# Kernel tuning notes

Measured on AMD Instinct MI355X. Metric: run time of the kernel, lower is better.

Reference implementation:

```python
import jax, jax.numpy as jnp
import numpy as np

B, N, D = 2, 2048, 1024
H, DH = 16, 64
EPS = 1e-5


def _layernorm(t, g, b):
    m = jnp.mean(t, axis=-1, keepdims=True)
    v = jnp.mean(jnp.square(t - m), axis=-1, keepdims=True)
    return (t - m) * jax.lax.rsqrt(v + EPS) * g + b


def setup_inputs() -> dict:
    key = jax.random.key(0)
    ks = jax.random.split(key, 4)
    return {
        "x": jax.random.normal(ks[0], (B, N, D), dtype=jnp.float32),
        "ln_g": jnp.ones((D,), jnp.float32),
        "ln_b": jnp.zeros((D,), jnp.float32),
        "lnc_g": jnp.ones((D,), jnp.float32),
        "lnc_b": jnp.zeros((D,), jnp.float32),
        "Wq": jax.random.normal(ks[1], (D, H * DH), jnp.float32) * 0.02,
        "Wkv": jax.random.normal(ks[2], (D, 2 * H * DH), jnp.float32) * 0.02,
        "Wo": jax.random.normal(ks[3], (H * DH, D), jnp.float32) * 0.02,
    }


def reference(x, ln_g, ln_b, lnc_g, lnc_b, Wq, Wkv, Wo):
    scale = DH ** (-0.5)
    xn = _layernorm(x, ln_g, ln_b)          # self-attn: context = x
    cn = _layernorm(x, lnc_g, lnc_b)
    q = xn @ Wq                              # [b, n, h*d]
    kv = cn @ Wkv
    k, v = jnp.split(kv, 2, axis=-1)
    # b n (h d) -> b h n d
    q = q.reshape(B, N, H, DH).transpose(0, 2, 1, 3)
    k = k.reshape(B, N, H, DH).transpose(0, 2, 1, 3)
    v = v.reshape(B, N, H, DH).transpose(0, 2, 1, 3)
    sim = jnp.einsum("bhnd,bhmd->bhnm", q, k) * scale
    neg = -jnp.finfo(sim.dtype).max
    causal = jnp.tril(jnp.ones((N, N), dtype=bool))  # allow j <= i
    sim = jnp.where(causal[None, None], sim, neg)
    attn = jax.nn.softmax(sim.astype(jnp.float32), axis=-1)
    out = jnp.einsum("bhnm,bhmd->bhnd", attn, v)
    out = out.transpose(0, 2, 1, 3).reshape(B, N, H * DH)
    return out @ Wo
```

## Files before the change

### kernel.cpp

```cpp
#include <hip/hip_runtime.h>
#include <hip/hip_bf16.h>

#define B_  2
#define N_  2048
#define D_  1024
#define H_  16
#define DH_ 64
#define BN_ROWS (B_ * N_)
#define EPS_ 1e-5f
#define QKV_N 3072

typedef __attribute__((ext_vector_type(8))) short bf16x8_t;
typedef __attribute__((ext_vector_type(4))) float f32x4_t;

typedef const unsigned int __attribute__((address_space(1)))* gas_ptr;
typedef unsigned int __attribute__((address_space(3)))* las_ptr;

__device__ __forceinline__ void async16(const unsigned short* g, unsigned short* l) {
    __builtin_amdgcn_global_load_lds((gas_ptr)g, (las_ptr)l, 16, 0, 0);
}

__device__ __forceinline__ unsigned short f2bf(float f) {
    unsigned int u = __float_as_uint(f);
    unsigned int r = u + 0x7FFFu + ((u >> 16) & 1u);
    return (unsigned short)(r >> 16);
}

__device__ __forceinline__ unsigned int pk2bf(float a, float b) {
    __hip_bfloat162 t = __float22bfloat162_rn(float2{a, b});
    return *(unsigned int*)&t;
}

__global__ __launch_bounds__(256) void ln_wt_kernel(
    const float* __restrict__ x,
    const float* __restrict__ g1, const float* __restrict__ b1,
    const float* __restrict__ g2, const float* __restrict__ b2,
    const float* __restrict__ Wq, const float* __restrict__ Wkv,
    const float* __restrict__ Wo,
    unsigned short* __restrict__ xn, unsigned short* __restrict__ cn,
    unsigned short* __restrict__ wqkvT, unsigned short* __restrict__ woT) {
    const int bid = blockIdx.x;
    const int tid = threadIdx.x;

    if (bid < BN_ROWS) {
        const int row = bid;
        const float4 v = ((const float4*)(x + (size_t)row * D_))[tid];

        float s  = v.x + v.y + v.z + v.w;
        float s2 = v.x * v.x + v.y * v.y + v.z * v.z + v.w * v.w;
        #pragma unroll
        for (int off = 32; off > 0; off >>= 1) {
            s  += __shfl_down(s,  off);
            s2 += __shfl_down(s2, off);
        }
        __shared__ float red[8];
        if ((tid & 63) == 0) { red[tid >> 6] = s; red[4 + (tid >> 6)] = s2; }
        __syncthreads();
        const float S  = red[0] + red[1] + red[2] + red[3];
        const float S2 = red[4] + red[5] + red[6] + red[7];
        const float mean = S * (1.0f / D_);
        const float var  = S2 * (1.0f / D_) - mean * mean;
        const float rstd = rsqrtf(var + EPS_);

        const float4 G1 = ((const float4*)g1)[tid];
        const float4 B1 = ((const float4*)b1)[tid];
        const float4 G2 = ((const float4*)g2)[tid];
        const float4 B2 = ((const float4*)b2)[tid];

        float nx[4] = { (v.x - mean) * rstd, (v.y - mean) * rstd,
                        (v.z - mean) * rstd, (v.w - mean) * rstd };
        ushort4 o1, o2;
        o1.x = f2bf(nx[0] * G1.x + B1.x); o1.y = f2bf(nx[1] * G1.y + B1.y);
        o1.z = f2bf(nx[2] * G1.z + B1.z); o1.w = f2bf(nx[3] * G1.w + B1.w);
        o2.x = f2bf(nx[0] * G2.x + B2.x); o2.y = f2bf(nx[1] * G2.y + B2.y);
        o2.z = f2bf(nx[2] * G2.z + B2.z); o2.w = f2bf(nx[3] * G2.w + B2.w);
        ((ushort4*)(xn + (size_t)row * D_))[tid] = o1;
        ((ushort4*)(cn + (size_t)row * D_))[tid] = o2;
    } else {
        const int zz = bid - BN_ROWS;
        const float* src;
        unsigned short* dst;
        int N, t;
        if (zz < 1024)      { src = Wq;  dst = wqkvT;                       N = 1024; t = zz; }
        else if (zz < 3072) { src = Wkv; dst = wqkvT + (size_t)1024 * 1024; N = 2048; t = zz - 1024; }
        else                { src = Wo;  dst = woT;                         N = 1024; t = zz - 3072; }
        const int nb = N / 32;
        const int n0 = (t % nb) * 32, k0 = (t / nb) * 32;

        __shared__ float tile[32][33];
        const int tx = tid & 31, ty = tid >> 5;
        #pragma unroll
        for (int i = 0; i < 4; i++)
            tile[ty + i * 8][tx] = src[(size_t)(k0 + ty + i * 8) * N + n0 + tx];
        __syncthreads();
        #pragma unroll
        for (int i = 0; i < 4; i++)
            dst[(size_t)(n0 + ty + i * 8) * 1024 + k0 + tx] = f2bf(tile[tx][ty + i * 8]);
    }
}

template <int BM, bool FUSED, bool BF16OUT, int MINW>
__global__ __launch_bounds__(256, MINW) void gemm_kernel(
    const unsigned short* __restrict__ A0, const unsigned short* __restrict__ A1,
    const unsigned short* __restrict__ Bt, void* __restrict__ Cv,
    unsigned short* __restrict__ vt, int M, int N, int K) {
    constexpr int WM = BM / 2, MT = WM / 16, AI = BM / 32;
    __shared__ unsigned short As[BM * 64];
    __shared__ unsigned short Bs[128 * 64];
    const int tid = threadIdx.x, lane = tid & 63, w = tid >> 6;
    const int quad = lane >> 4, l16 = lane & 15;
    const int lr8 = lane >> 3, pg8 = lane & 7;
    const int wr = (w >> 1) * WM, wc = (w & 1) * 64;
    const int bm = blockIdx.y * BM, bn = blockIdx.x * 128;
    const unsigned short* A = (FUSED && bn >= 1024) ? A1 : A0;
    const float cscale = (FUSED && bn < 1024) ? 0.180336880111120f : 1.0f;

    f32x4_t acc[MT][4] = {};
    for (int k0 = 0; k0 < K; k0 += 64) {
        #pragma unroll
        for (int i = 0; i < AI; i++) {
            const int rb = w * (BM / 4) + i * 8;
            const int r  = rb + lr8;
            const int g  = pg8 ^ (r & 7);
            async16(&A[(size_t)(bm + r) * K + k0 + g * 8], &As[rb * 64]);
        }
        #pragma unroll
        for (int i = 0; i < 4; i++) {
            const int rb = w * 32 + i * 8;
            const int r  = rb + lr8;
            const int g  = pg8 ^ (r & 7);
            async16(&Bt[(size_t)(bn + r) * K + k0 + g * 8], &Bs[rb * 64]);
        }
        __syncthreads();
        #pragma unroll
        for (int kk = 0; kk < 64; kk += 32) {
            bf16x8_t af[MT], bfr[4];
            const int g0 = (kk >> 3) + quad;
            #pragma unroll
            for (int t = 0; t < MT; t++)
                af[t] = *(const bf16x8_t*)&As[(wr + t * 16 + l16) * 64 +
                                              ((g0 ^ (l16 & 7)) * 8)];
            #pragma unroll
            for (int t = 0; t < 4; t++)
                bfr[t] = *(const bf16x8_t*)&Bs[(wc + t * 16 + l16) * 64 +
                                               ((g0 ^ (l16 & 7)) * 8)];
            #pragma unroll
            for (int mt = 0; mt < MT; mt++)
                #pragma unroll
                for (int nt = 0; nt < 4; nt++)
                    acc[mt][nt] = __builtin_amdgcn_mfma_f32_16x16x32_bf16(
                        af[mt], bfr[nt], acc[mt][nt], 0, 0, 0);
        }
        __syncthreads();
    }

    if (FUSED && bn >= 2048) {
        const int seq0 = bm + wr;
        const int bq = seq0 >> 11;
        const int kt = (seq0 & (N_ - 1)) >> 6;
        #pragma unroll
        for (int nt = 0; nt < 4; nt++) {
            const int c = (bn - 2048) + wc + nt * 16 + l16;
            unsigned short* dst =
                vt + (((size_t)(bq * 32 + kt) * 1024) + c) * 64;
            #pragma unroll
            for (int mt = 0; mt < 4; mt++) {
                uint2 v2 = { pk2bf(acc[mt][nt][0], acc[mt][nt][1]),
                             pk2bf(acc[mt][nt][2], acc[mt][nt][3]) };
                *(uint2*)&dst[mt * 16 + quad * 4] = v2;
            }
        }
        return;
    }

    #pragma unroll
    for (int mt = 0; mt < MT; mt++)
        #pragma unroll
        for (int nt = 0; nt < 4; nt++)
            #pragma unroll
            for (int r = 0; r < 4; r++) {
                const int row = bm + wr + mt * 16 + quad * 4 + r;
                const int col = bn + wc + nt * 16 + l16;
                if (BF16OUT)
                    ((unsigned short*)Cv)[(size_t)row * N + col] =
                        f2bf(acc[mt][nt][r] * cscale);
                else
                    ((float*)Cv)[(size_t)row * N + col] = acc[mt][nt][r];
            }
}

__global__ __launch_bounds__(256, 3) void flash_attn_kernel(
    const unsigned short* __restrict__ qkv, const unsigned short* __restrict__ vt,
    unsigned short* __restrict__ out) {
    __shared__ unsigned short Qs[64 * 64];
    __shared__ unsigned short Ks[2][64 * 64];
    __shared__ unsigned short Vts[2][64 * 64];
    __shared__ unsigned short Ps[4][16 * 72];

    const int tid = threadIdx.x, lane = tid & 63, w = tid >> 6;
    const int quad = lane >> 4, l16 = lane & 15;
    const int lr8 = lane >> 3, pg8 = lane & 7;
    const int bid = blockIdx.x;
    const int b5  = bid & 31;
    const int bh  = (b5 & 7) * 4 + (b5 >> 3);
    const int qt  = 31 - (bid >> 5);
    const int b = bh >> 4, h = bh & 15;
    const int qs = qt * 64;
    const int niter = qt + 1;

    const unsigned short* qb  = qkv + (size_t)(b * N_) * QKV_N + h * DH_;
    const unsigned short* kb  = qb + 1024;
    const unsigned short* vtb = vt + ((size_t)(b * 32) * 1024 + h * 64) * 64;

    bf16x8_t ones;
    #pragma unroll
    for (int j = 0; j < 8; j++) ones[j] = (short)0x3F80;

    const int r0 = w * 16 + lr8;
    const int r1 = r0 + 8;
    const int g0s = pg8 ^ (r0 & 7);
    const int g1s = pg8 ^ (r1 & 7);
    const unsigned short* kp0 = &kb[(size_t)r0 * QKV_N + g0s * 8];
    const unsigned short* kp1 = &kb[(size_t)r1 * QKV_N + g1s * 8];
    const unsigned short* vp0 = &vtb[(size_t)r0 * 64 + g0s * 8];
    const unsigned short* vp1 = &vtb[(size_t)r1 * 64 + g1s * 8];
    const int rb0 = w * 16, rb1 = w * 16 + 8;

    async16(&qb[(size_t)(qs + r0) * QKV_N + g0s * 8], &Qs[rb0 * 64]);
    async16(&qb[(size_t)(qs + r1) * QKV_N + g1s * 8], &Qs[rb1 * 64]);
    async16(kp0, &Ks[0][rb0 * 64]);
    async16(kp1, &Ks[0][rb1 * 64]);
    async16(vp0, &Vts[0][rb0 * 64]);
    async16(vp1, &Vts[0][rb1 * 64]);
    __syncthreads();

    bf16x8_t qf[2];
    #pragma unroll
    for (int k2 = 0; k2 < 2; k2++) {
        const int gq = k2 * 4 + quad;
        qf[k2] = *(const bf16x8_t*)&Qs[(w * 16 + l16) * 64 + ((gq ^ (l16 & 7)) * 8)];
    }

    int ksoff[2][4], vtoff[2][4], psoff[2];
    #pragma unroll
    for (int k2 = 0; k2 < 2; k2++) {
        const int gq = k2 * 4 + quad;
        #pragma unroll
        for (int t = 0; t < 4; t++) {
            ksoff[k2][t] = (t * 16 + l16) * 64 + ((gq ^ (l16 & 7)) * 8);
            vtoff[k2][t] = ksoff[k2][t];
        }
        psoff[k2] = l16 * 72 + k2 * 32 + quad * 8;
    }
    const int qy = qs + w * 16 + l16;

    f32x4_t o[4] = {};
    f32x4_t lacc = {};

    for (int jt = 0; jt < niter; jt++) {
        if (jt) __syncthreads();

        if (jt + 1 < niter) {
            const size_t koff = (size_t)(jt + 1) * 64 * QKV_N;
            const size_t voff = (size_t)(jt + 1) * 1024 * 64;
            const int bsel = (jt + 1) & 1;
            async16(kp0 + koff, &Ks[bsel][rb0 * 64]);
            async16(kp1 + koff, &Ks[bsel][rb1 * 64]);
            async16(vp0 + voff, &Vts[bsel][rb0 * 64]);
            async16(vp1 + voff, &Vts[bsel][rb1 * 64]);
        }
        const int buf = jt & 1;
        const int js = jt * 64;

        f32x4_t s[4] = {};
        #pragma unroll
        for (int k2 = 0; k2 < 2; k2++)
            #pragma unroll
            for (int kt = 0; kt < 4; kt++) {
                const bf16x8_t a = *(const bf16x8_t*)&Ks[buf][ksoff[k2][kt]];
                s[kt] = __builtin_amdgcn_mfma_f32_16x16x32_bf16(
                    a, qf[k2], s[kt], 0, 0, 0);
            }

        const bool edge = (jt == niter - 1);
        #pragma unroll
        for (int kt = 0; kt < 4; kt++) {
            float p[4];
            #pragma unroll
            for (int r = 0; r < 4; r++) {
                float sv = s[kt][r];
                if (edge && (js + kt * 16 + quad * 4 + r > qy)) sv = -3e38f;
                p[r] = exp2f(sv);
            }
            uint2 pk = { pk2bf(p[0], p[1]), pk2bf(p[2], p[3]) };
            *(uint2*)&Ps[w][l16 * 72 + kt * 16 + quad * 4] = pk;
        }

        #pragma unroll
        for (int k2 = 0; k2 < 2; k2++) {
            const bf16x8_t ap = *(const bf16x8_t*)&Ps[w][psoff[k2]];
            #pragma unroll
            for (int nt = 0; nt < 4; nt++) {
                const bf16x8_t bv = *(const bf16x8_t*)&Vts[buf][vtoff[k2][nt]];
                o[nt] = __builtin_amdgcn_mfma_f32_16x16x32_bf16(
                    ap, bv, o[nt], 0, 0, 0);
            }
            lacc = __builtin_amdgcn_mfma_f32_16x16x32_bf16(
                ap, ones, lacc, 0, 0, 0);
        }
    }

    #pragma unroll
    for (int r = 0; r < 4; r++) {
        const float inv = 1.0f / lacc[r];
        const int query = qs + w * 16 + quad * 4 + r;
        const int row = b * N_ + query;
        #pragma unroll
        for (int nt = 0; nt < 4; nt++) {
            const int col = h * DH_ + nt * 16 + l16;
            out[(size_t)row * (H_ * DH_) + col] = f2bf(o[nt][r] * inv);
        }
    }
}

extern "C" void kernel_launch(void* const* d_in, const int* in_sizes, int n_in,
                              void* d_out, int out_size, void* d_ws, size_t ws_size,
                              hipStream_t stream) {
    const float* x     = (const float*)d_in[0];
    const float* ln_g  = (const float*)d_in[1];
    const float* ln_b  = (const float*)d_in[2];
    const float* lnc_g = (const float*)d_in[3];
    const float* lnc_b = (const float*)d_in[4];
    const float* Wq    = (const float*)d_in[5];
    const float* Wkv   = (const float*)d_in[6];
    const float* Wo    = (const float*)d_in[7];

    char* ws = (char*)d_ws;
    const size_t MB = 1024 * 1024;
    unsigned short* qkv   = (unsigned short*)(ws + 0 * MB);
    unsigned short* vtbuf = (unsigned short*)(ws + 24 * MB);
    unsigned short* xn    = (unsigned short*)(ws + 32 * MB);
    unsigned short* cn    = (unsigned short*)(ws + 40 * MB);
    unsigned short* wqkvT = (unsigned short*)(ws + 48 * MB);
    unsigned short* woT   = (unsigned short*)(ws + 54 * MB);
    unsigned short* ao    = xn;

    ln_wt_kernel<<<8192, 256, 0, stream>>>(
        x, ln_g, ln_b, lnc_g, lnc_b, Wq, Wkv, Wo, xn, cn, wqkvT, woT);

    gemm_kernel<128, true, true, 3>
        <<<dim3(QKV_N / 128, BN_ROWS / 128), 256, 0, stream>>>(
        xn, cn, wqkvT, qkv, vtbuf, BN_ROWS, QKV_N, D_);

    flash_attn_kernel<<<B_ * H_ * 32, 256, 0, stream>>>(qkv, vtbuf, ao);

    gemm_kernel<64, false, false, 2>
        <<<dim3(D_ / 128, BN_ROWS / 64), 256, 0, stream>>>(
        ao, nullptr, woT, (float*)d_out, nullptr, BN_ROWS, D_, H_ * DH_);
}
```

Measured before the change: 182.8 us.

## Pair complementary causal query tiles per block to balance work and share K/V

Each attention block now handles two query tiles, p and 31-p, so every block does roughly the same number of causal key iterations and each K/V tile loaded into LDS serves both query tiles. The grid is halved, the P scratch buffer is aliased onto the Q staging area after the Q fragments are moved to registers, and launch bounds drop to 2 blocks per SM. This removes the causal tail imbalance and halves K/V loads per query, in exchange for more registers (two accumulator sets) and fewer resident blocks.

Result: slower. 190.5 us (+4.2%).

```diff
diff --git a/kernel.cpp b/kernel.cpp
--- a/kernel.cpp
+++ b/kernel.cpp
@@ -189,13 +189,12 @@
             }
 }
 
-__global__ __launch_bounds__(256, 3) void flash_attn_kernel(
+__global__ __launch_bounds__(256, 2) void flash_attn_kernel(
     const unsigned short* __restrict__ qkv, const unsigned short* __restrict__ vt,
     unsigned short* __restrict__ out) {
-    __shared__ unsigned short Qs[64 * 64];
+    __shared__ unsigned short Qs[2][64 * 64];
     __shared__ unsigned short Ks[2][64 * 64];
     __shared__ unsigned short Vts[2][64 * 64];
-    __shared__ unsigned short Ps[4][16 * 72];
 
     const int tid = threadIdx.x, lane = tid & 63, w = tid >> 6;
     const int quad = lane >> 4, l16 = lane & 15;
@@ -203,10 +202,11 @@
     const int bid = blockIdx.x;
     const int b5  = bid & 31;
     const int bh  = (b5 & 7) * 4 + (b5 >> 3);
-    const int qt  = 31 - (bid >> 5);
+    const int p   = bid >> 5;
     const int b = bh >> 4, h = bh & 15;
-    const int qs = qt * 64;
-    const int niter = qt + 1;
+    const int qtA = p, qtB = 31 - p;
+    const int qsA = qtA * 64, qsB = qtB * 64;
+    const int niter = qtB + 1;
 
     const unsigned short* qb  = qkv + (size_t)(b * N_) * QKV_N + h * DH_;
     const unsigned short* kb  = qb + 1024;
@@ -216,46 +216,45 @@
     #pragma unroll
     for (int j = 0; j < 8; j++) ones[j] = (short)0x3F80;
 
-    const int r0 = w * 16 + lr8;
-    const int r1 = r0 + 8;
-    const int g0s = pg8 ^ (r0 & 7);
-    const int g1s = pg8 ^ (r1 & 7);
+    const int r0 = w * 16 + lr8, r1 = r0 + 8;
+    const int g0s = pg8 ^ (r0 & 7), g1s = pg8 ^ (r1 & 7);
+    const int rb0 = w * 16, rb1 = rb0 + 8;
     const unsigned short* kp0 = &kb[(size_t)r0 * QKV_N + g0s * 8];
     const unsigned short* kp1 = &kb[(size_t)r1 * QKV_N + g1s * 8];
     const unsigned short* vp0 = &vtb[(size_t)r0 * 64 + g0s * 8];
     const unsigned short* vp1 = &vtb[(size_t)r1 * 64 + g1s * 8];
-    const int rb0 = w * 16, rb1 = w * 16 + 8;
-
-    async16(&qb[(size_t)(qs + r0) * QKV_N + g0s * 8], &Qs[rb0 * 64]);
-    async16(&qb[(size_t)(qs + r1) * QKV_N + g1s * 8], &Qs[rb1 * 64]);
+
+    async16(&qb[(size_t)(qsA + r0) * QKV_N + g0s * 8], &Qs[0][rb0 * 64]);
+    async16(&qb[(size_t)(qsA + r1) * QKV_N + g1s * 8], &Qs[0][rb1 * 64]);
+    async16(&qb[(size_t)(qsB + r0) * QKV_N + g0s * 8], &Qs[1][rb0 * 64]);
+    async16(&qb[(size_t)(qsB + r1) * QKV_N + g1s * 8], &Qs[1][rb1 * 64]);
     async16(kp0, &Ks[0][rb0 * 64]);
     async16(kp1, &Ks[0][rb1 * 64]);
     async16(vp0, &Vts[0][rb0 * 64]);
     async16(vp1, &Vts[0][rb1 * 64]);
     __syncthreads();
 
-    bf16x8_t qf[2];
+    bf16x8_t qfA[2], qfB[2];
+    int fragoff[2][4], psoff[2];
     #pragma unroll
     for (int k2 = 0; k2 < 2; k2++) {
         const int gq = k2 * 4 + quad;
-        qf[k2] = *(const bf16x8_t*)&Qs[(w * 16 + l16) * 64 + ((gq ^ (l16 & 7)) * 8)];
-    }
-
-    int ksoff[2][4], vtoff[2][4], psoff[2];
-    #pragma unroll
-    for (int k2 = 0; k2 < 2; k2++) {
-        const int gq = k2 * 4 + quad;
-        #pragma unroll
-        for (int t = 0; t < 4; t++) {
-            ksoff[k2][t] = (t * 16 + l16) * 64 + ((gq ^ (l16 & 7)) * 8);
-            vtoff[k2][t] = ksoff[k2][t];
-        }
+        const int qo = (w * 16 + l16) * 64 + ((gq ^ (l16 & 7)) * 8);
+        qfA[k2] = *(const bf16x8_t*)&Qs[0][qo];
+        qfB[k2] = *(const bf16x8_t*)&Qs[1][qo];
+        #pragma unroll
+        for (int t = 0; t < 4; t++)
+            fragoff[k2][t] = (t * 16 + l16) * 64 + ((gq ^ (l16 & 7)) * 8);
         psoff[k2] = l16 * 72 + k2 * 32 + quad * 8;
     }
-    const int qy = qs + w * 16 + l16;
-
-    f32x4_t o[4] = {};
-    f32x4_t lacc = {};
+    __syncthreads();
+
+    unsigned short* Psw = &Qs[0][0] + w * (16 * 72);
+    const int qyA = qsA + w * 16 + l16;
+    const int qyB = qsB + w * 16 + l16;
+
+    f32x4_t oA[4] = {}, oB[4] = {};
+    f32x4_t lA = {}, lB = {};
 
     for (int jt = 0; jt < niter; jt++) {
         if (jt) __syncthreads();
@@ -271,54 +270,97 @@
         }
         const int buf = jt & 1;
         const int js = jt * 64;
-
-        f32x4_t s[4] = {};
+        const bool actA = (jt <= p);
+
+        f32x4_t sA[4] = {}, sB[4] = {};
+        if (actA) {
+            #pragma unroll
+            for (int k2 = 0; k2 < 2; k2++)
+                #pragma unroll
+                for (int kt = 0; kt < 4; kt++) {
+                    const bf16x8_t a = *(const bf16x8_t*)&Ks[buf][fragoff[k2][kt]];
+                    sB[kt] = __builtin_amdgcn_mfma_f32_16x16x32_bf16(a, qfB[k2], sB[kt], 0, 0, 0);
+                    sA[kt] = __builtin_amdgcn_mfma_f32_16x16x32_bf16(a, qfA[k2], sA[kt], 0, 0, 0);
+                }
+        } else {
+            #pragma unroll
+            for (int k2 = 0; k2 < 2; k2++)
+                #pragma unroll
+                for (int kt = 0; kt < 4; kt++) {
+                    const bf16x8_t a = *(const bf16x8_t*)&Ks[buf][fragoff[k2][kt]];
+                    sB[kt] = __builtin_amdgcn_mfma_f32_16x16x32_bf16(a, qfB[k2], sB[kt], 0, 0, 0);
+                }
+        }
+
+        bf16x8_t bv[2][4];
         #pragma unroll
         for (int k2 = 0; k2 < 2; k2++)
             #pragma unroll
+            for (int nt = 0; nt < 4; nt++)
+                bv[k2][nt] = *(const bf16x8_t*)&Vts[buf][fragoff[k2][nt]];
+
+        {
+            const bool edge = (jt == qtB);
+            #pragma unroll
             for (int kt = 0; kt < 4; kt++) {
-                const bf16x8_t a = *(const bf16x8_t*)&Ks[buf][ksoff[k2][kt]];
-                s[kt] = __builtin_amdgcn_mfma_f32_16x16x32_bf16(
-                    a, qf[k2], s[kt], 0, 0, 0);
-            }
-
-        const bool edge = (jt == niter - 1);
-        #pragma unroll
-        for (int kt = 0; kt < 4; kt++) {
-            float p[4];
-            #pragma unroll
-            for (int r = 0; r < 4; r++) {
-                float sv = s[kt][r];
-                if (edge && (js + kt * 16 + quad * 4 + r > qy)) sv = -3e38f;
-                p[r] = exp2f(sv);
-            }
-            uint2 pk = { pk2bf(p[0], p[1]), pk2bf(p[2], p[3]) };
-            *(uint2*)&Ps[w][l16 * 72 + kt * 16 + quad * 4] = pk;
-        }
-
-        #pragma unroll
-        for (int k2 = 0; k2 < 2; k2++) {
-            const bf16x8_t ap = *(const bf16x8_t*)&Ps[w][psoff[k2]];
-            #pragma unroll
-            for (int nt = 0; nt < 4; nt++) {
-                const bf16x8_t bv = *(const bf16x8_t*)&Vts[buf][vtoff[k2][nt]];
-                o[nt] = __builtin_amdgcn_mfma_f32_16x16x32_bf16(
-                    ap, bv, o[nt], 0, 0, 0);
-            }
-            lacc = __builtin_amdgcn_mfma_f32_16x16x32_bf16(
-                ap, ones, lacc, 0, 0, 0);
+                float pv[4];
+                #pragma unroll
+                for (int r = 0; r < 4; r++) {
+                    float sv = sB[kt][r];
+                    if (edge && (js + kt * 16 + quad * 4 + r > qyB)) sv = -3e38f;
+                    pv[r] = exp2f(sv);
+                }
+                uint2 pk = { pk2bf(pv[0], pv[1]), pk2bf(pv[2], pv[3]) };
+                *(uint2*)&Psw[l16 * 72 + kt * 16 + quad * 4] = pk;
+            }
+            #pragma unroll
+            for (int k2 = 0; k2 < 2; k2++) {
+                const bf16x8_t ap = *(const bf16x8_t*)&Psw[psoff[k2]];
+                #pragma unroll
+                for (int nt = 0; nt < 4; nt++)
+                    oB[nt] = __builtin_amdgcn_mfma_f32_16x16x32_bf16(
+                        ap, bv[k2][nt], oB[nt], 0, 0, 0);
+                lB = __builtin_amdgcn_mfma_f32_16x16x32_bf16(ap, ones, lB, 0, 0, 0);
+            }
+        }
+
+        if (actA) {
+            const bool edge = (jt == qtA);
+            #pragma unroll
+            for (int kt = 0; kt < 4; kt++) {
+                float pv[4];
+                #pragma unroll
+                for (int r = 0; r < 4; r++) {
+                    float sv = sA[kt][r];
+                    if (edge && (js + kt * 16 + quad * 4 + r > qyA)) sv = -3e38f;
+                    pv[r] = exp2f(sv);
+                }
+                uint2 pk = { pk2bf(pv[0], pv[1]), pk2bf(pv[2], pv[3]) };
+                *(uint2*)&Psw[l16 * 72 + kt * 16 + quad * 4] = pk;
+            }
+            #pragma unroll
+            for (int k2 = 0; k2 < 2; k2++) {
+                const bf16x8_t ap = *(const bf16x8_t*)&Psw[psoff[k2]];
+                #pragma unroll
+                for (int nt = 0; nt < 4; nt++)
+                    oA[nt] = __builtin_amdgcn_mfma_f32_16x16x32_bf16(
+                        ap, bv[k2][nt], oA[nt], 0, 0, 0);
+                lA = __builtin_amdgcn_mfma_f32_16x16x32_bf16(ap, ones, lA, 0, 0, 0);
+            }
         }
     }
 
     #pragma unroll
     for (int r = 0; r < 4; r++) {
-        const float inv = 1.0f / lacc[r];
-        const int query = qs + w * 16 + quad * 4 + r;
-        const int row = b * N_ + query;
+        const float invA = 1.0f / lA[r];
+        const float invB = 1.0f / lB[r];
+        const int rowA = b * N_ + qsA + w * 16 + quad * 4 + r;
+        const int rowB = b * N_ + qsB + w * 16 + quad * 4 + r;
         #pragma unroll
         for (int nt = 0; nt < 4; nt++) {
             const int col = h * DH_ + nt * 16 + l16;
-            out[(size_t)row * (H_ * DH_) + col] = f2bf(o[nt][r] * inv);
+            out[(size_t)rowA * (H_ * DH_) + col] = f2bf(oA[nt][r] * invA);
+            out[(size_t)rowB * (H_ * DH_) + col] = f2bf(oB[nt][r] * invB);
         }
     }
 }
@@ -352,7 +394,7 @@
         <<<dim3(QKV_N / 128, BN_ROWS / 128), 256, 0, stream>>>(
         xn, cn, wqkvT, qkv, vtbuf, BN_ROWS, QKV_N, D_);
 
-    flash_attn_kernel<<<B_ * H_ * 32, 256, 0, stream>>>(qkv, vtbuf, ao);
+    flash_attn_kernel<<<B_ * H_ * 16, 256, 0, stream>>>(qkv, vtbuf, ao);
 
     gemm_kernel<64, false, false, 2>
         <<<dim3(D_ / 128, BN_ROWS / 64), 256, 0, stream>>>(
```

## Enlarge flash-attention query tile to 128 rows per block with balanced scheduling

Applied to the files above, without the earlier changes.

Each attention block now handles 128 query rows instead of 64, and each wave computes two 16-row query fragments, so every K/V tile loaded into LDS and every K/V fragment read is reused across twice as many queries. The grid halves to 512 blocks, and the block-to-tile mapping pairs short and long causal rows (qt = a or 15-a) to balance work. It gives up occupancy (launch bounds 3 to 2, larger LDS and register footprint) and applies masking over two diagonal iterations instead of one.

Measured after the change: 201.2 us. 1.1x slower.

```diff
diff --git a/kernel.cpp b/kernel.cpp
--- a/kernel.cpp
+++ b/kernel.cpp
@@ -189,24 +189,26 @@
             }
 }
 
-__global__ __launch_bounds__(256, 3) void flash_attn_kernel(
+__global__ __launch_bounds__(256, 2) void flash_attn_kernel(
     const unsigned short* __restrict__ qkv, const unsigned short* __restrict__ vt,
     unsigned short* __restrict__ out) {
-    __shared__ unsigned short Qs[64 * 64];
+    __shared__ unsigned short Qs[128 * 64];
     __shared__ unsigned short Ks[2][64 * 64];
     __shared__ unsigned short Vts[2][64 * 64];
-    __shared__ unsigned short Ps[4][16 * 72];
+    __shared__ unsigned short Ps[4][32 * 72];
 
     const int tid = threadIdx.x, lane = tid & 63, w = tid >> 6;
     const int quad = lane >> 4, l16 = lane & 15;
     const int lr8 = lane >> 3, pg8 = lane & 7;
+
     const int bid = blockIdx.x;
-    const int b5  = bid & 31;
-    const int bh  = (b5 & 7) * 4 + (b5 >> 3);
-    const int qt  = 31 - (bid >> 5);
+    const int c   = bid & 255, hi = bid >> 8;
+    const int bh  = (c & 7) * 4 + ((c >> 3) & 3);
+    const int a   = c >> 5;
+    const int qt  = hi ? (15 - a) : a;
     const int b = bh >> 4, h = bh & 15;
-    const int qs = qt * 64;
-    const int niter = qt + 1;
+    const int qs = qt * 128;
+    const int niter = 2 * qt + 2;
 
     const unsigned short* qb  = qkv + (size_t)(b * N_) * QKV_N + h * DH_;
     const unsigned short* kb  = qb + 1024;
@@ -216,46 +218,44 @@
     #pragma unroll
     for (int j = 0; j < 8; j++) ones[j] = (short)0x3F80;
 
-    const int r0 = w * 16 + lr8;
-    const int r1 = r0 + 8;
-    const int g0s = pg8 ^ (r0 & 7);
-    const int g1s = pg8 ^ (r1 & 7);
+    const int r0 = w * 16 + lr8, r1 = r0 + 8;
+    const int g0s = pg8 ^ (r0 & 7), g1s = pg8 ^ (r1 & 7);
+    const int rb0 = w * 16, rb1 = rb0 + 8;
     const unsigned short* kp0 = &kb[(size_t)r0 * QKV_N + g0s * 8];
     const unsigned short* kp1 = &kb[(size_t)r1 * QKV_N + g1s * 8];
     const unsigned short* vp0 = &vtb[(size_t)r0 * 64 + g0s * 8];
     const unsigned short* vp1 = &vtb[(size_t)r1 * 64 + g1s * 8];
-    const int rb0 = w * 16, rb1 = w * 16 + 8;
-
-    async16(&qb[(size_t)(qs + r0) * QKV_N + g0s * 8], &Qs[rb0 * 64]);
-    async16(&qb[(size_t)(qs + r1) * QKV_N + g1s * 8], &Qs[rb1 * 64]);
+
+    #pragma unroll
+    for (int i = 0; i < 4; i++) {
+        const int rb = w * 32 + i * 8;
+        const int r  = rb + lr8;
+        const int g  = pg8 ^ (r & 7);
+        async16(&qb[(size_t)(qs + r) * QKV_N + g * 8], &Qs[rb * 64]);
+    }
     async16(kp0, &Ks[0][rb0 * 64]);
     async16(kp1, &Ks[0][rb1 * 64]);
     async16(vp0, &Vts[0][rb0 * 64]);
     async16(vp1, &Vts[0][rb1 * 64]);
     __syncthreads();
 
-    bf16x8_t qf[2];
+    bf16x8_t qf[2][2];
+    int fragoff[2][4], psoff[2];
     #pragma unroll
     for (int k2 = 0; k2 < 2; k2++) {
         const int gq = k2 * 4 + quad;
-        qf[k2] = *(const bf16x8_t*)&Qs[(w * 16 + l16) * 64 + ((gq ^ (l16 & 7)) * 8)];
-    }
-
-    int ksoff[2][4], vtoff[2][4], psoff[2];
-    #pragma unroll
-    for (int k2 = 0; k2 < 2; k2++) {
-        const int gq = k2 * 4 + quad;
-        #pragma unroll
-        for (int t = 0; t < 4; t++) {
-            ksoff[k2][t] = (t * 16 + l16) * 64 + ((gq ^ (l16 & 7)) * 8);
-            vtoff[k2][t] = ksoff[k2][t];
-        }
+        #pragma unroll
+        for (int nq = 0; nq < 2; nq++)
+            qf[nq][k2] = *(const bf16x8_t*)&Qs[
+                (w * 32 + nq * 16 + l16) * 64 + ((gq ^ (l16 & 7)) * 8)];
+        #pragma unroll
+        for (int t = 0; t < 4; t++)
+            fragoff[k2][t] = (t * 16 + l16) * 64 + ((gq ^ (l16 & 7)) * 8);
         psoff[k2] = l16 * 72 + k2 * 32 + quad * 8;
     }
-    const int qy = qs + w * 16 + l16;
-
-    f32x4_t o[4] = {};
-    f32x4_t lacc = {};
+
+    f32x4_t o[2][4] = {};
+    f32x4_t lacc[2] = {};
 
     for (int jt = 0; jt < niter; jt++) {
         if (jt) __syncthreads();
@@ -272,55 +272,70 @@
         const int buf = jt & 1;
         const int js = jt * 64;
 
-        f32x4_t s[4] = {};
+        f32x4_t s[4][2] = {};
         #pragma unroll
         for (int k2 = 0; k2 < 2; k2++)
             #pragma unroll
             for (int kt = 0; kt < 4; kt++) {
-                const bf16x8_t a = *(const bf16x8_t*)&Ks[buf][ksoff[k2][kt]];
-                s[kt] = __builtin_amdgcn_mfma_f32_16x16x32_bf16(
-                    a, qf[k2], s[kt], 0, 0, 0);
-            }
-
-        const bool edge = (jt == niter - 1);
-        #pragma unroll
-        for (int kt = 0; kt < 4; kt++) {
-            float p[4];
-            #pragma unroll
-            for (int r = 0; r < 4; r++) {
-                float sv = s[kt][r];
-                if (edge && (js + kt * 16 + quad * 4 + r > qy)) sv = -3e38f;
-                p[r] = exp2f(sv);
-            }
-            uint2 pk = { pk2bf(p[0], p[1]), pk2bf(p[2], p[3]) };
-            *(uint2*)&Ps[w][l16 * 72 + kt * 16 + quad * 4] = pk;
+                const bf16x8_t aK = *(const bf16x8_t*)&Ks[buf][fragoff[k2][kt]];
+                #pragma unroll
+                for (int nq = 0; nq < 2; nq++)
+                    s[kt][nq] = __builtin_amdgcn_mfma_f32_16x16x32_bf16(
+                        aK, qf[nq][k2], s[kt][nq], 0, 0, 0);
+            }
+
+        const bool edge = (jt >= niter - 2);
+        #pragma unroll
+        for (int nq = 0; nq < 2; nq++) {
+            const int qy = qs + w * 32 + nq * 16 + l16;
+            #pragma unroll
+            for (int kt = 0; kt < 4; kt++) {
+                float pv[4];
+                #pragma unroll
+                for (int r = 0; r < 4; r++) {
+                    float sv = s[kt][nq][r];
+                    if (edge && (js + kt * 16 + quad * 4 + r > qy)) sv = -3e38f;
+                    pv[r] = exp2f(sv);
+                }
+                uint2 pk = { pk2bf(pv[0], pv[1]), pk2bf(pv[2], pv[3]) };
+                *(uint2*)&Ps[w][(nq * 16 + l16) * 72 + kt * 16 + quad * 4] = pk;
+            }
         }
 
         #pragma unroll
         for (int k2 = 0; k2 < 2; k2++) {
-            const bf16x8_t ap = *(const bf16x8_t*)&Ps[w][psoff[k2]];
+            bf16x8_t ap[2];
+            #pragma unroll
+            for (int mq = 0; mq < 2; mq++)
+                ap[mq] = *(const bf16x8_t*)&Ps[w][(mq * 16 + l16) * 72 +
+                                                  k2 * 32 + quad * 8];
             #pragma unroll
             for (int nt = 0; nt < 4; nt++) {
-                const bf16x8_t bv = *(const bf16x8_t*)&Vts[buf][vtoff[k2][nt]];
-                o[nt] = __builtin_amdgcn_mfma_f32_16x16x32_bf16(
-                    ap, bv, o[nt], 0, 0, 0);
-            }
-            lacc = __builtin_amdgcn_mfma_f32_16x16x32_bf16(
-                ap, ones, lacc, 0, 0, 0);
-        }
-    }
-
-    #pragma unroll
-    for (int r = 0; r < 4; r++) {
-        const float inv = 1.0f / lacc[r];
-        const int query = qs + w * 16 + quad * 4 + r;
-        const int row = b * N_ + query;
-        #pragma unroll
-        for (int nt = 0; nt < 4; nt++) {
-            const int col = h * DH_ + nt * 16 + l16;
-            out[(size_t)row * (H_ * DH_) + col] = f2bf(o[nt][r] * inv);
-        }
-    }
+                const bf16x8_t bv = *(const bf16x8_t*)&Vts[buf][fragoff[k2][nt]];
+                #pragma unroll
+                for (int mq = 0; mq < 2; mq++)
+                    o[mq][nt] = __builtin_amdgcn_mfma_f32_16x16x32_bf16(
+                        ap[mq], bv, o[mq][nt], 0, 0, 0);
+            }
+            #pragma unroll
+            for (int mq = 0; mq < 2; mq++)
+                lacc[mq] = __builtin_amdgcn_mfma_f32_16x16x32_bf16(
+                    ap[mq], ones, lacc[mq], 0, 0, 0);
+        }
+    }
+
+    #pragma unroll
+    for (int mq = 0; mq < 2; mq++)
+        #pragma unroll
+        for (int r = 0; r < 4; r++) {
+            const float inv = 1.0f / lacc[mq][r];
+            const int row = b * N_ + qs + w * 32 + mq * 16 + quad * 4 + r;
+            #pragma unroll
+            for (int nt = 0; nt < 4; nt++) {
+                const int col = h * DH_ + nt * 16 + l16;
+                out[(size_t)row * (H_ * DH_) + col] = f2bf(o[mq][nt][r] * inv);
+            }
+        }
 }
 
 extern "C" void kernel_launch(void* const* d_in, const int* in_sizes, int n_in,
@@ -352,7 +367,7 @@
         <<<dim3(QKV_N / 128, BN_ROWS / 128), 256, 0, stream>>>(
         xn, cn, wqkvT, qkv, vtbuf, BN_ROWS, QKV_N, D_);
 
-    flash_attn_kernel<<<B_ * H_ * 32, 256, 0, stream>>>(qkv, vtbuf, ao);
+    flash_attn_kernel<<<512, 256, 0, stream>>>(qkv, vtbuf, ao);
 
     gemm_kernel<64, false, false, 2>
         <<<dim3(D_ / 128, BN_ROWS / 64), 256, 0, stream>>>(
```
